# Kernel tuning notes

Measured on AMD Instinct MI355X. Metric: run time of the kernel, lower is better.

## Reference

```python
import jax, jax.numpy as jnp
import numpy as np

NUM_HEADS = 8
WINDOW = 7
DILATION = 1
EPS = 1e-5


def channel_ln(x, w, b):
    # x: [B, C, H, W]; normalize over channel dim (axis=1)
    mu = jnp.mean(x, axis=1, keepdims=True)
    var = jnp.var(x, axis=1, keepdims=True)
    xhat = (x - mu) * jax.lax.rsqrt(var + EPS)
    return xhat * w[None, :, None, None] + b[None, :, None, None]


def local_mask(H, W, window, dilation):
    r = (window // 2) * dilation
    ii, jj = jnp.meshgrid(jnp.arange(H), jnp.arange(W), indexing="ij")
    ii = ii.reshape(-1)
    jj = jj.reshape(-1)
    di = jnp.abs(ii[:, None] - ii[None, :])
    dj = jnp.abs(jj[:, None] - jj[None, :])
    m = (di <= r) & (dj <= r)
    if dilation > 1:
        m = m & (di % dilation == 0) & (dj % dilation == 0)
    return m  # [N, N] bool


def local_attention(x, qkv_w, qkv_b, proj_w, proj_b):
    B, C, H, W = x.shape
    N = H * W
    hd = C // NUM_HEADS
    t = x.reshape(B, C, N).transpose(0, 2, 1)            # [B, N, C]
    qkv = t @ qkv_w.T + qkv_b                            # [B, N, 3C]
    qkv = qkv.reshape(B, N, 3, NUM_HEADS, hd)
    q, k, v = (qkv[:, :, i].transpose(0, 2, 1, 3) for i in range(3))  # [B,h,N,d]
    scale = 1.0 / jnp.sqrt(jnp.asarray(hd, x.dtype))
    scores = jnp.einsum("bhnd,bhmd->bhnm", q, k) * scale  # [B,h,N,N]
    mask = local_mask(H, W, WINDOW, DILATION)             # [N,N]
    scores = jnp.where(mask[None, None], scores, jnp.asarray(-jnp.inf, x.dtype))
    attn = jax.nn.softmax(scores, axis=-1)
    out = jnp.einsum("bhnm,bhmd->bhnd", attn, v)          # [B,h,N,d]
    out = out.transpose(0, 2, 1, 3).reshape(B, N, C)      # [B,N,C]
    out = out @ proj_w.T + proj_b
    return out.transpose(0, 2, 1).reshape(B, C, H, W)


def mlp2d(x, fc1_w, fc1_b, fc2_w, fc2_b):
    # 1x1 convs == per-pixel linear over channels
    h = jnp.einsum("bchw,oc->bohw", x, fc1_w) + fc1_b[None, :, None, None]
    h = jax.nn.gelu(h, approximate=False)
    return jnp.einsum("bchw,oc->bohw", h, fc2_w) + fc2_b[None, :, None, None]


def setup_inputs() -> dict:
    key = jax.random.key(0)
    ks = jax.random.split(key, 12)
    B, C, H, W = 1, 256, 56, 56
    hidden = 4 * C
    s = lambda fan: 1.0 / np.sqrt(fan)
    return {
        "x": jax.random.normal(ks[0], (B, C, H, W), jnp.float32),
        "norm1_w": jnp.ones((C,), jnp.float32),
        "norm1_b": jnp.zeros((C,), jnp.float32),
        "qkv_w": jax.random.normal(ks[1], (3 * C, C), jnp.float32) * s(C),
        "qkv_b": jnp.zeros((3 * C,), jnp.float32),
        "proj_w": jax.random.normal(ks[2], (C, C), jnp.float32) * s(C),
        "proj_b": jnp.zeros((C,), jnp.float32),
        "norm2_w": jnp.ones((C,), jnp.float32),
        "norm2_b": jnp.zeros((C,), jnp.float32),
        "fc1_w": jax.random.normal(ks[3], (hidden, C), jnp.float32) * s(C),
        "fc1_b": jnp.zeros((hidden,), jnp.float32),
        "fc2_w": jax.random.normal(ks[4], (C, hidden), jnp.float32) * s(hidden),
        "fc2_b": jnp.zeros((C,), jnp.float32),
    }


def reference(x, norm1_w, norm1_b, qkv_w, qkv_b, proj_w, proj_b,
              norm2_w, norm2_b, fc1_w, fc1_b, fc2_w, fc2_b):
    x = x + local_attention(channel_ln(x, norm1_w, norm1_b), qkv_w, qkv_b, proj_w, proj_b)
    x = x + mlp2d(channel_ln(x, norm2_w, norm2_b), fc1_w, fc1_b, fc2_w, fc2_b)
    return x
```

## Files before the change

### kernel.cpp

```cpp
#include <hip/hip_runtime.h>
#include <math.h>


typedef unsigned int uint;
typedef unsigned short ushort;
typedef unsigned long long u64;
typedef __attribute__((ext_vector_type(8))) short short8;
typedef __attribute__((ext_vector_type(4))) float floatx4;
typedef __attribute__((ext_vector_type(4))) unsigned short ushort4v;

#define AS1(p) (const __attribute__((address_space(1))) void*)(p)
#define AS3(p) (__attribute__((address_space(3))) void*)(p)

__device__ __forceinline__ float bf2f(ushort u) {
  union { uint i; float f; } v; v.i = ((uint)u) << 16; return v.f;
}
__device__ __forceinline__ ushort f2bf(float f) {
  union { float f; uint i; } v; v.f = f;
  uint u = v.i;
  return (ushort)((u + 0x7fffu + ((u >> 16) & 1u)) >> 16);
}

__device__ __forceinline__ void stage64(const ushort* src, int kstride,
                                        ushort* dstBase, int tid) {
  const int srow = tid >> 5;
  const int scb  = (tid & 31) ^ srow;
  const ushort* g = src + (size_t)srow * kstride + scb * 8;
  ushort* d = dstBase + tid * 8;
  #pragma unroll
  for (int r = 0; r < 8; ++r) {
    __builtin_amdgcn_global_load_lds(AS1(g), AS3(d), 16, 0, 0);
    g += 8 * kstride;
    d += 2048;
  }
}

__device__ __forceinline__ void compute64(const ushort* As, const ushort* Bs,
                                          int w, int lane, floatx4 acc[4]) {
  const int fm = lane & 15;
  const int q  = lane >> 4;
  const int swz = fm & 7;
  const int arow = (w * 16 + fm) * 256;
  #pragma unroll
  for (int kt = 0; kt < 8; ++kt) {
    const int blk = ((kt * 4 + q) ^ swz) * 8;
    short8 af = *(const short8*)&As[arow + blk];
    #pragma unroll
    for (int nt = 0; nt < 4; ++nt) {
      short8 bfr = *(const short8*)&Bs[(nt * 16 + fm) * 256 + blk];
      acc[nt] = __builtin_amdgcn_mfma_f32_16x16x32_bf16(af, bfr, acc[nt], 0, 0, 0);
    }
  }
}

__global__ __launch_bounds__(256) void prep_kernel(
    const float* __restrict__ x, const float* __restrict__ n1w,
    const float* __restrict__ n1b,
    const float* __restrict__ qkvw, const float* __restrict__ projw,
    const float* __restrict__ f1w, const float* __restrict__ f2w,
    float* __restrict__ xT, ushort* __restrict__ t1, ushort* __restrict__ wcat)
{
  const int tid = threadIdx.x;
  const int bid = blockIdx.x;
  if (bid >= 196) {
    int idx = (bid - 196) * 256 + tid;
    float v;
    if (idx < 196608)       v = qkvw[idx];
    else if (idx < 262144)  v = projw[idx - 196608];
    else if (idx < 524288)  v = f1w[idx - 262144];
    else                    v = f2w[idx - 524288];
    wcat[idx] = f2bf(v);
    return;
  }
  __shared__ float tile[256 * 17];
  __shared__ float red[2][16][16];
  __shared__ float mu[16], rsv[16];
  const int n0 = bid * 16;
  const int px = tid & 15, grp = tid >> 4;
  #pragma unroll 4
  for (int it = 0; it < 16; ++it) {
    int c = it * 16 + grp;
    tile[c * 17 + px] = x[(size_t)c * 3136 + n0 + px];
  }
  __syncthreads();
  float s = 0.f, ss = 0.f;
  #pragma unroll
  for (int i = 0; i < 16; ++i) {
    float v = tile[(grp * 16 + i) * 17 + px];
    s += v; ss += v * v;
  }
  red[0][px][grp] = s; red[1][px][grp] = ss;
  __syncthreads();
  if (tid < 16) {
    float s2 = 0.f, ss2 = 0.f;
    #pragma unroll
    for (int g = 0; g < 16; ++g) { s2 += red[0][tid][g]; ss2 += red[1][tid][g]; }
    float m = s2 * (1.f / 256.f);
    float var = ss2 * (1.f / 256.f) - m * m;
    mu[tid] = m;
    rsv[tid] = rsqrtf(var + 1e-5f);
  }
  __syncthreads();
  const float wc = n1w[tid], bc = n1b[tid];
  #pragma unroll 4
  for (int p = 0; p < 16; ++p) {
    float v = tile[tid * 17 + p];
    xT[(size_t)(n0 + p) * 256 + tid] = v;
    t1[(size_t)(n0 + p) * 256 + tid] = f2bf((v - mu[p]) * rsv[p] * wc + bc);
  }
}

__global__ __launch_bounds__(256, 2) void qkv_kernel(
    const ushort* __restrict__ A, const ushort* __restrict__ B,
    const float* __restrict__ bias, ushort* __restrict__ out)
{
  __shared__ ushort As[16384], Bs[16384];
  const int tid = threadIdx.x, lane = tid & 63, w = tid >> 6;
  const int m0 = blockIdx.y * 64, n0 = blockIdx.x * 64;
  floatx4 acc[4] = {{0.f,0.f,0.f,0.f},{0.f,0.f,0.f,0.f},
                    {0.f,0.f,0.f,0.f},{0.f,0.f,0.f,0.f}};
  stage64(A + (size_t)m0 * 256, 256, As, tid);
  stage64(B + (size_t)n0 * 256, 256, Bs, tid);
  asm volatile("s_waitcnt vmcnt(0)" ::: "memory");
  __syncthreads();
  compute64(As, Bs, w, lane, acc);
  const int fm = lane & 15, q4 = (lane >> 4) * 4;
  #pragma unroll
  for (int nt = 0; nt < 4; ++nt)
    #pragma unroll
    for (int r = 0; r < 4; ++r) {
      int m = m0 + w * 16 + q4 + r;
      int n = n0 + nt * 16 + fm;
      float v = acc[nt][r] + bias[n];
      if (n < 256) v *= 0.17677669529663687f;
      out[(size_t)m * 768 + n] = f2bf(v);
    }
}

#define AM_SMEM 144448

__global__ __launch_bounds__(512, 1) void attnmlp_kernel(
    const ushort* __restrict__ qkv, const ushort* __restrict__ pw_bf,
    const float* __restrict__ projb, const float* __restrict__ xT,
    const ushort* __restrict__ f1_bf, const float* __restrict__ f1b,
    const ushort* __restrict__ f2_bf, const float* __restrict__ f2b,
    const float* __restrict__ n2w, const float* __restrict__ n2b,
    float* __restrict__ outf)
{
  __shared__ __align__(16) char smem[AM_SMEM];
  ushort* Kh    = (ushort*)smem;
  ushort* Vh    = (ushort*)(smem + 52000);
  float*  pr    = (float*)(smem + 103200);
  ushort* aas   = (ushort*)(smem + 136000);
  ushort* pslab = (ushort*)smem;
  float*  x1s   = (float*)(smem + 103200);
  ushort* hbuf  = (ushort*)smem;
  ushort* fslab = (ushort*)(smem + 32768);
  ushort* t2s   = (ushort*)(smem + 120096);
  float*  pstat = (float*)(smem + 128288);
  float*  stats = (float*)(smem + 129312);

  const int tid = threadIdx.x;
  const int wv = tid >> 6, lane = tid & 63;
  const int fm = lane & 15, q = lane >> 4;
  const int l4 = lane >> 2, lb = lane & 3;
  const int i0 = (blockIdx.x / 14) * 4, j0 = (blockIdx.x % 14) * 4;

  for (int s = tid; s < 3200; s += 512) {
    int p = s >> 5, ck = s & 31;
    int ii = i0 - 3 + p / 10, jj = j0 - 3 + p % 10;
    if (ii >= 0 && ii < 56 && jj >= 0 && jj < 56) {
      const ushort* kr = qkv + (size_t)(ii * 56 + jj) * 768 + 256 + ck * 8;
      short8 kv = *(const short8*)kr;
      u64 lo = ((const u64*)&kv)[0], hi = ((const u64*)&kv)[1];
      *(u64*)&Kh[p * 260 + ck * 8] = lo;
      *(u64*)&Kh[p * 260 + ck * 8 + 4] = hi;
      *(short8*)&Vh[p * 256 + ck * 8] = *(const short8*)(kr + 256);
    } else {
      *(u64*)&Kh[p * 260 + ck * 8] = 0ull;
      *(u64*)&Kh[p * 260 + ck * 8 + 4] = 0ull;
      short8 z = {0, 0, 0, 0, 0, 0, 0, 0};
      *(short8*)&Vh[p * 256 + ck * 8] = z;
    }
  }
  __syncthreads();

  {
    const int h = lane >> 3, mg = lane & 7;
    #pragma unroll
    for (int qq = 0; qq < 2; ++qq) {
      const int p = wv * 2 + qq;
      const int qi = p >> 2, qj = p & 3;
      const int iq = i0 + qi, jq = j0 + qj;
      const ushort* qp = qkv + (size_t)(iq * 56 + jq) * 768 + h * 32;
      float qf[32];
      #pragma unroll
      for (int u = 0; u < 4; ++u) {
        short8 qv = *(const short8*)(qp + u * 8);
        #pragma unroll
        for (int e = 0; e < 8; ++e) qf[u * 8 + e] = bf2f((ushort)qv[e]);
      }
      float sv[7];
      float mx = -1e30f;
      #pragma unroll
      for (int k = 0; k < 7; ++k) {
        int m = mg + 8 * k;
        float s = -1e30f;
        if (m < 49) {
          int mi = m / 7, mj = m % 7;
          int ii = iq + mi - 3, jj = jq + mj - 3;
          if (ii >= 0 && ii < 56 && jj >= 0 && jj < 56) {
            int hrow = (qi + mi) * 10 + (qj + mj);
            const u64* k8 = (const u64*)&Kh[hrow * 260 + h * 32];
            float a = 0.f;
            #pragma unroll
            for (int u = 0; u < 8; ++u) {
              u64 kv = k8[u];
              #pragma unroll
              for (int e = 0; e < 4; ++e)
                a += qf[u * 4 + e] * bf2f((ushort)(kv >> (16 * e)));
            }
            s = a;
          }
        }
        sv[k] = s;
        mx = fmaxf(mx, s);
      }
      mx = fmaxf(mx, __shfl_xor(mx, 1));
      mx = fmaxf(mx, __shfl_xor(mx, 2));
      mx = fmaxf(mx, __shfl_xor(mx, 4));
      float sm = 0.f;
      #pragma unroll
      for (int k = 0; k < 7; ++k) { sv[k] = __expf(sv[k] - mx); sm += sv[k]; }
      sm += __shfl_xor(sm, 1);
      sm += __shfl_xor(sm, 2);
      sm += __shfl_xor(sm, 4);
      float inv = 1.f / sm;
      #pragma unroll
      for (int k = 0; k < 7; ++k) {
        int m = mg + 8 * k;
        pr[(p * 8 + h) * 64 + m] = sv[k] * inv;
      }
    }
  }
  __syncthreads();

  ushort* ps0 = pslab + wv * 2048;
  ushort* ps1 = ps0 + 1024;
#define STAGE_P(kt, buf) do { \
    _Pragma("unroll") \
    for (int i_ = 0; i_ < 2; ++i_) { \
      int row_ = i_ * 16 + l4; \
      const ushort* g_ = pw_bf + (size_t)(wv * 32 + row_) * 256 + (kt) * 32 + (lb ^ (row_ & 3)) * 8; \
      __builtin_amdgcn_global_load_lds(AS1(g_), AS3((buf) + i_ * 512 + lane * 8), 16, 0, 0); \
    } } while (0)
  STAGE_P(0, ps0);

  {
    const int p = tid >> 5, cg = tid & 31, hh = cg >> 2;
    const int qi = p >> 2, qj = p & 3;
    float acc8[8] = {0, 0, 0, 0, 0, 0, 0, 0};
    #pragma unroll
    for (int mi = 0; mi < 7; ++mi)
      #pragma unroll
      for (int mj = 0; mj < 7; ++mj) {
        int m = mi * 7 + mj;
        int hrow = (qi + mi) * 10 + (qj + mj);
        float pm = pr[(p * 8 + hh) * 64 + m];
        short8 v8 = *(const short8*)&Vh[hrow * 256 + cg * 8];
        #pragma unroll
        for (int e = 0; e < 8; ++e)
          acc8[e] += pm * bf2f((ushort)v8[e]);
      }
    short8 o;
    #pragma unroll
    for (int e = 0; e < 8; ++e) o[e] = (short)f2bf(acc8[e]);
    *(short8*)&aas[p * 264 + cg * 8] = o;
  }
  __syncthreads();

  {
    floatx4 pacc[2] = {{0.f,0.f,0.f,0.f},{0.f,0.f,0.f,0.f}};
    for (int kt = 0; kt < 8; ++kt) {
      ushort* cur = (kt & 1) ? ps1 : ps0;
      ushort* nxt = (kt & 1) ? ps0 : ps1;
      if (kt < 7) {
        STAGE_P(kt + 1, nxt);
        asm volatile("s_waitcnt vmcnt(2)" ::: "memory");
      } else {
        asm volatile("s_waitcnt vmcnt(0)" ::: "memory");
      }
      short8 af = *(const short8*)&aas[fm * 264 + kt * 32 + q * 8];
      #pragma unroll
      for (int nt = 0; nt < 2; ++nt) {
        int r = nt * 16 + fm;
        short8 bfr = *(const short8*)&cur[r * 32 + (q ^ (r & 3)) * 8];
        pacc[nt] = __builtin_amdgcn_mfma_f32_16x16x32_bf16(af, bfr, pacc[nt], 0, 0, 0);
      }
    }
    #pragma unroll
    for (int nt = 0; nt < 2; ++nt) {
      int ch = wv * 32 + nt * 16 + fm;
      #pragma unroll
      for (int r = 0; r < 4; ++r) {
        int px = q * 4 + r;
        int n = (i0 + (px >> 2)) * 56 + j0 + (px & 3);
        x1s[px * 264 + ch] = pacc[nt][r] + projb[ch] + xT[(size_t)n * 256 + ch];
      }
    }
  }
  ushort* fs0 = fslab + wv * 4096;
  ushort* fs1 = fs0 + 2048;
#define STAGE_F1(c, kt, buf) do { \
    _Pragma("unroll") \
    for (int i_ = 0; i_ < 4; ++i_) { \
      int row_ = i_ * 16 + l4; \
      const ushort* g_ = f1_bf + (size_t)((c) * 64 + row_) * 256 + (kt) * 32 + (lb ^ (row_ & 3)) * 8; \
      __builtin_amdgcn_global_load_lds(AS1(g_), AS3((buf) + i_ * 512 + lane * 8), 16, 0, 0); \
    } } while (0)
  STAGE_F1(wv, 0, fs0);
  __syncthreads();

  floatx4 xv[2];
  xv[0] = *(const floatx4*)&x1s[fm * 264 + wv * 32 + q * 4];
  xv[1] = *(const floatx4*)&x1s[fm * 264 + wv * 32 + 16 + q * 4];
  {
    float s = 0.f, ss = 0.f;
    #pragma unroll
    for (int nt = 0; nt < 2; ++nt)
      #pragma unroll
      for (int e = 0; e < 4; ++e) { s += xv[nt][e]; ss += xv[nt][e] * xv[nt][e]; }
    s += __shfl_xor(s, 16); ss += __shfl_xor(ss, 16);
    s += __shfl_xor(s, 32); ss += __shfl_xor(ss, 32);
    if (lane < 16) { pstat[(wv * 16 + lane) * 2] = s; pstat[(wv * 16 + lane) * 2 + 1] = ss; }
  }
  __syncthreads();
  if (tid < 16) {
    float s2 = 0.f, ss2 = 0.f;
    #pragma unroll
    for (int ww = 0; ww < 8; ++ww) {
      s2 += pstat[(ww * 16 + tid) * 2];
      ss2 += pstat[(ww * 16 + tid) * 2 + 1];
    }
    float mu = s2 * (1.f / 256.f);
    float var = ss2 * (1.f / 256.f) - mu * mu;
    stats[tid * 2] = mu;
    stats[tid * 2 + 1] = rsqrtf(var + 1e-5f);
  }
  __syncthreads();
  {
    float mu = stats[fm * 2], rs = stats[fm * 2 + 1];
    #pragma unroll
    for (int nt = 0; nt < 2; ++nt) {
      int ch0 = wv * 32 + nt * 16 + q * 4;
      ushort4v o;
      #pragma unroll
      for (int e = 0; e < 4; ++e)
        o[e] = f2bf((xv[nt][e] - mu) * rs * n2w[ch0 + e] + n2b[ch0 + e]);
      int slot = ch0 >> 3;
      *(ushort4v*)&t2s[fm * 256 + ((slot ^ (fm & 7)) * 8) + (ch0 & 7)] = o;
    }
  }
  float f1br[2][4];
  #pragma unroll
  for (int ci = 0; ci < 2; ++ci)
    #pragma unroll
    for (int nt = 0; nt < 4; ++nt)
      f1br[ci][nt] = f1b[(wv + ci * 8) * 64 + nt * 16 + fm];
  __syncthreads();

  {
    floatx4 fa[4] = {{0.f,0.f,0.f,0.f},{0.f,0.f,0.f,0.f},
                     {0.f,0.f,0.f,0.f},{0.f,0.f,0.f,0.f}};
    for (int sidx = 0; sidx < 16; ++sidx) {
      const int kt = sidx & 7;
      const int ci = sidx >> 3;
      ushort* cur = (sidx & 1) ? fs1 : fs0;
      ushort* nxt = (sidx & 1) ? fs0 : fs1;
      if (sidx < 15) {
        int s1 = sidx + 1;
        STAGE_F1(wv + (s1 >> 3) * 8, s1 & 7, nxt);
        asm volatile("s_waitcnt vmcnt(4)" ::: "memory");
      } else {
        asm volatile("s_waitcnt vmcnt(0)" ::: "memory");
      }
      short8 af = *(const short8*)&t2s[fm * 256 + (((kt * 4 + q) ^ (fm & 7)) * 8)];
      #pragma unroll
      for (int nt = 0; nt < 4; ++nt) {
        int r = nt * 16 + fm;
        short8 bfr = *(const short8*)&cur[r * 32 + (q ^ (r & 3)) * 8];
        fa[nt] = __builtin_amdgcn_mfma_f32_16x16x32_bf16(af, bfr, fa[nt], 0, 0, 0);
      }
      if (kt == 7) {
        #pragma unroll
        for (int nt = 0; nt < 4; ++nt) {
          int hc = (wv + ci * 8) * 64 + nt * 16 + fm;
          #pragma unroll
          for (int r4 = 0; r4 < 4; ++r4) {
            int prow = q * 4 + r4;
            float v = fa[nt][r4] + f1br[ci][nt];
            v = 0.5f * v * (1.0f + erff(v * 0.70710678118654752f));
            hbuf[prow * 1024 + (((hc >> 3) ^ (prow & 7)) * 8) + (hc & 7)] = f2bf(v);
            fa[nt][r4] = 0.f;
          }
        }
      }
    }
  }
  ushort* gs0 = fs0;
  ushort* gs1 = fs0 + 1024;
#define STAGE_F2(kt, buf) do { \
    _Pragma("unroll") \
    for (int i_ = 0; i_ < 2; ++i_) { \
      int row_ = i_ * 16 + l4; \
      const ushort* g_ = f2_bf + (size_t)(wv * 32 + row_) * 1024 + (kt) * 32 + (lb ^ (row_ & 3)) * 8; \
      __builtin_amdgcn_global_load_lds(AS1(g_), AS3((buf) + i_ * 512 + lane * 8), 16, 0, 0); \
    } } while (0)
  STAGE_F2(0, gs0);
  __syncthreads();

  {
    floatx4 ga[2] = {{0.f,0.f,0.f,0.f},{0.f,0.f,0.f,0.f}};
    for (int kt = 0; kt < 32; ++kt) {
      ushort* cur = (kt & 1) ? gs1 : gs0;
      ushort* nxt = (kt & 1) ? gs0 : gs1;
      if (kt < 31) {
        STAGE_F2(kt + 1, nxt);
        asm volatile("s_waitcnt vmcnt(2)" ::: "memory");
      } else {
        asm volatile("s_waitcnt vmcnt(0)" ::: "memory");
      }
      short8 bfr = *(const short8*)&hbuf[fm * 1024 + (((kt * 4 + q) ^ (fm & 7)) * 8)];
      #pragma unroll
      for (int mt = 0; mt < 2; ++mt) {
        int r = mt * 16 + fm;
        short8 af = *(const short8*)&cur[r * 32 + (q ^ (r & 3)) * 8];
        ga[mt] = __builtin_amdgcn_mfma_f32_16x16x32_bf16(af, bfr, ga[mt], 0, 0, 0);
      }
    }
    #pragma unroll
    for (int mt = 0; mt < 2; ++mt) {
      #pragma unroll
      for (int r4 = 0; r4 < 4; ++r4) {
        int ch = wv * 32 + mt * 16 + q * 4 + r4;
        int n = (i0 + (fm >> 2)) * 56 + j0 + (fm & 3);
        outf[(size_t)ch * 3136 + n] = ga[mt][r4] + f2b[ch] + xv[mt][r4];
      }
    }
  }
#undef STAGE_P
#undef STAGE_F1
#undef STAGE_F2
}

extern "C" void kernel_launch(void* const* d_in, const int* in_sizes, int n_in,
                              void* d_out, int out_size, void* d_ws, size_t ws_size,
                              hipStream_t stream) {
  const float* x     = (const float*)d_in[0];
  const float* n1w   = (const float*)d_in[1];
  const float* n1b   = (const float*)d_in[2];
  const float* qkvw  = (const float*)d_in[3];
  const float* qkvb  = (const float*)d_in[4];
  const float* projw = (const float*)d_in[5];
  const float* projb = (const float*)d_in[6];
  const float* n2w   = (const float*)d_in[7];
  const float* n2b   = (const float*)d_in[8];
  const float* f1w   = (const float*)d_in[9];
  const float* f1b   = (const float*)d_in[10];
  const float* f2w   = (const float*)d_in[11];
  const float* f2b   = (const float*)d_in[12];

  char* ws = (char*)d_ws;
  ushort* wcat = (ushort*)(ws + 0);
  float*  xT   = (float*)(ws + 1572864);
  ushort* t    = (ushort*)(ws + 4784128);
  ushort* qh   = (ushort*)(ws + 6389760);

  const ushort* qw_bf = wcat;
  const ushort* pw_bf = wcat + 196608;
  const ushort* f1_bf = wcat + 262144;
  const ushort* f2_bf = wcat + 524288;
  float* outf = (float*)d_out;

  hipLaunchKernelGGL(prep_kernel, dim3(3268), dim3(256), 0, stream,
                     x, n1w, n1b, qkvw, projw, f1w, f2w, xT, t, wcat);
  hipLaunchKernelGGL(qkv_kernel, dim3(12, 49), dim3(256), 0, stream,
                     t, qw_bf, qkvb, qh);
  hipLaunchKernelGGL(attnmlp_kernel, dim3(196), dim3(512), 0, stream,
                     qh, pw_bf, projb, xT, f1_bf, f1b, f2_bf, f2b,
                     n2w, n2b, outf);
}
```

Before: 126.3 us.

## Move weight conversion into qkv kernel, drop xT buffer, pad prob rows

The conversion of the proj/fc1/fc2 weights to bf16 moves from the prep kernel into extra blocks of the qkv GEMM launch. Only the qkv weights are still converted in prep, so prep becomes shorter ahead of the dependent GEMM. The transposed fp32 copy of x (xT) is no longer written; the attention kernel reads the residual straight from x in NCHW layout with a float4 load. The attention-probability rows in shared memory are padded from 64 to 67 floats to reduce bank conflicts. The extra blocks lengthen the qkv launch, and the residual read now strides across channels.

```diff
diff --git a/kernel.cpp b/kernel.cpp
--- a/kernel.cpp
+++ b/kernel.cpp
@@ -55,21 +55,14 @@
 
 __global__ __launch_bounds__(256) void prep_kernel(
     const float* __restrict__ x, const float* __restrict__ n1w,
-    const float* __restrict__ n1b,
-    const float* __restrict__ qkvw, const float* __restrict__ projw,
-    const float* __restrict__ f1w, const float* __restrict__ f2w,
-    float* __restrict__ xT, ushort* __restrict__ t1, ushort* __restrict__ wcat)
+    const float* __restrict__ n1b, const float* __restrict__ qkvw,
+    ushort* __restrict__ t1, ushort* __restrict__ wcat)
 {
   const int tid = threadIdx.x;
   const int bid = blockIdx.x;
   if (bid >= 196) {
     int idx = (bid - 196) * 256 + tid;
-    float v;
-    if (idx < 196608)       v = qkvw[idx];
-    else if (idx < 262144)  v = projw[idx - 196608];
-    else if (idx < 524288)  v = f1w[idx - 262144];
-    else                    v = f2w[idx - 524288];
-    wcat[idx] = f2bf(v);
+    wcat[idx] = f2bf(qkvw[idx]);
     return;
   }
   __shared__ float tile[256 * 17];
@@ -105,17 +98,29 @@
   #pragma unroll 4
   for (int p = 0; p < 16; ++p) {
     float v = tile[tid * 17 + p];
-    xT[(size_t)(n0 + p) * 256 + tid] = v;
     t1[(size_t)(n0 + p) * 256 + tid] = f2bf((v - mu[p]) * rsv[p] * wc + bc);
   }
 }
 
 __global__ __launch_bounds__(256, 2) void qkv_kernel(
     const ushort* __restrict__ A, const ushort* __restrict__ B,
-    const float* __restrict__ bias, ushort* __restrict__ out)
+    const float* __restrict__ bias, ushort* __restrict__ out,
+    const float* __restrict__ projw, const float* __restrict__ f1w,
+    const float* __restrict__ f2w, ushort* __restrict__ wcat)
 {
+  const int tid = threadIdx.x;
+  if (blockIdx.y >= 49) {
+    int c = (blockIdx.y - 49) * 12 + blockIdx.x;
+    int idx = c * 256 + tid;
+    float v;
+    if (idx < 65536)        v = projw[idx];
+    else if (idx < 327680)  v = f1w[idx - 65536];
+    else                    v = f2w[idx - 327680];
+    wcat[196608 + idx] = f2bf(v);
+    return;
+  }
   __shared__ ushort As[16384], Bs[16384];
-  const int tid = threadIdx.x, lane = tid & 63, w = tid >> 6;
+  const int lane = tid & 63, w = tid >> 6;
   const int m0 = blockIdx.y * 64, n0 = blockIdx.x * 64;
   floatx4 acc[4] = {{0.f,0.f,0.f,0.f},{0.f,0.f,0.f,0.f},
                     {0.f,0.f,0.f,0.f},{0.f,0.f,0.f,0.f}};
@@ -137,11 +142,11 @@
     }
 }
 
-#define AM_SMEM 144448
+#define AM_SMEM 145952
 
 __global__ __launch_bounds__(512, 1) void attnmlp_kernel(
     const ushort* __restrict__ qkv, const ushort* __restrict__ pw_bf,
-    const float* __restrict__ projb, const float* __restrict__ xT,
+    const float* __restrict__ projb, const float* __restrict__ x,
     const ushort* __restrict__ f1_bf, const float* __restrict__ f1b,
     const ushort* __restrict__ f2_bf, const float* __restrict__ f2b,
     const float* __restrict__ n2w, const float* __restrict__ n2b,
@@ -151,7 +156,7 @@
   ushort* Kh    = (ushort*)smem;
   ushort* Vh    = (ushort*)(smem + 52000);
   float*  pr    = (float*)(smem + 103200);
-  ushort* aas   = (ushort*)(smem + 136000);
+  ushort* aas   = (ushort*)(smem + 137504);
   ushort* pslab = (ushort*)smem;
   float*  x1s   = (float*)(smem + 103200);
   ushort* hbuf  = (ushort*)smem;
@@ -239,7 +244,7 @@
       #pragma unroll
       for (int k = 0; k < 7; ++k) {
         int m = mg + 8 * k;
-        pr[(p * 8 + h) * 64 + m] = sv[k] * inv;
+        pr[(p * 8 + h) * 67 + m] = sv[k] * inv;
       }
     }
   }
@@ -266,7 +271,7 @@
       for (int mj = 0; mj < 7; ++mj) {
         int m = mi * 7 + mj;
         int hrow = (qi + mi) * 10 + (qj + mj);
-        float pm = pr[(p * 8 + hh) * 64 + m];
+        float pm = pr[(p * 8 + hh) * 67 + m];
         short8 v8 = *(const short8*)&Vh[hrow * 256 + cg * 8];
         #pragma unroll
         for (int e = 0; e < 8; ++e)
@@ -301,11 +306,11 @@
     #pragma unroll
     for (int nt = 0; nt < 2; ++nt) {
       int ch = wv * 32 + nt * 16 + fm;
+      floatx4 rx = *(const floatx4*)(x + (size_t)ch * 3136 + (i0 + q) * 56 + j0);
       #pragma unroll
       for (int r = 0; r < 4; ++r) {
         int px = q * 4 + r;
-        int n = (i0 + (px >> 2)) * 56 + j0 + (px & 3);
-        x1s[px * 264 + ch] = pacc[nt][r] + projb[ch] + xT[(size_t)n * 256 + ch];
+        x1s[px * 264 + ch] = pacc[nt][r] + projb[ch] + rx[r];
       }
     }
   }
@@ -472,7 +477,6 @@
 
   char* ws = (char*)d_ws;
   ushort* wcat = (ushort*)(ws + 0);
-  float*  xT   = (float*)(ws + 1572864);
   ushort* t    = (ushort*)(ws + 4784128);
   ushort* qh   = (ushort*)(ws + 6389760);
 
@@ -482,11 +486,11 @@
   const ushort* f2_bf = wcat + 524288;
   float* outf = (float*)d_out;
 
-  hipLaunchKernelGGL(prep_kernel, dim3(3268), dim3(256), 0, stream,
-                     x, n1w, n1b, qkvw, projw, f1w, f2w, xT, t, wcat);
-  hipLaunchKernelGGL(qkv_kernel, dim3(12, 49), dim3(256), 0, stream,
-                     t, qw_bf, qkvb, qh);
+  hipLaunchKernelGGL(prep_kernel, dim3(964), dim3(256), 0, stream,
+                     x, n1w, n1b, qkvw, t, wcat);
+  hipLaunchKernelGGL(qkv_kernel, dim3(12, 241), dim3(256), 0, stream,
+                     t, qw_bf, qkvb, qh, projw, f1w, f2w, wcat);
   hipLaunchKernelGGL(attnmlp_kernel, dim3(196), dim3(512), 0, stream,
-                     qh, pw_bf, projb, xT, f1_bf, f1b, f2_bf, f2b,
+                     qh, pw_bf, projb, x, f1_bf, f1b, f2_bf, f2b,
                      n2w, n2b, outf);
 }
```

Result: no change. 125.9 us (-0.4%).
